# Optimization experiments

Measured on AMD Instinct MI355X. Metric: run time of the kernel, lower is better.

## Reference

```python
import jax, jax.numpy as jnp
import numpy as np

UNITS = 4096                                # number of heap nodes (power of two)
DEPTH = (UNITS - 1).bit_length() + 1        # 13 heap steps (k = 0..12)
FEATURES = [2, 64, 64, 2]
BATCH = 256


def _build_heap_maps(nodes):
    """For each heap step k, precompute for every output node j the input
    (ancestor) node index it reads from, plus a validity mask. This encodes
    exactly the torch block loop: for level l, input nodes [floor(2^(l-1)), 2^l)
    broadcast (repeat_interleave by heap_factor) into output range
    [out_node0, out_node1), with blocks where out_node1 > nodes skipped."""
    depth = (nodes - 1).bit_length() + 1
    maps = []
    for k in range(depth):
        idx = np.zeros(nodes, np.int32)
        mask = np.zeros(nodes, np.bool_)
        for l in range(depth):
            in0 = 0 if l == 0 else 2 ** (l - 1)
            if in0 == 0:  # root block (node 0)
                hf = 1 if k == 0 else 2 ** (k - 1)      # ceil(2^(k-1))
                out0 = 0 if k == 0 else 2 ** (k - 1)    # floor(2^(k-1))
                out1 = out0 + hf
            else:
                hf = 2 ** k
                out0 = in0 * hf
                out1 = (2 ** l) * hf
            if out1 <= nodes:
                js = np.arange(out0, out1)
                idx[js] = in0 + (js - out0) // hf
                mask[js] = True
        maps.append((jnp.asarray(idx), jnp.asarray(mask)))
    return maps


MAPS = _build_heap_maps(UNITS)


def heap_linear(x, W, b, minheap):
    # x: [..., nodes, in_f]; W: [K, out_f, in_f]; b: [K, out_f]; K = DEPTH - minheap
    out = jnp.zeros(x.shape[:-1] + (W.shape[1],), jnp.float32)
    for i, k in enumerate(range(minheap, DEPTH)):
        idx, mask = MAPS[k]
        # apply linear_k to every node once, then gather parent -> children
        y = jnp.einsum('...ni,oi->...no', x, W[i]) + b[i]
        out = out + jnp.where(mask[:, None], y[..., idx, :], 0.0)
    return out


def setup_inputs() -> dict:
    key = jax.random.key(0)
    ks = jax.random.split(key, 7)
    f0, f1, f2, f3 = FEATURES

    def w(k, n, o, i):
        return jax.random.normal(k, (n, o, i), jnp.float32) / np.float32(np.sqrt(i))

    return {
        "x": jax.random.normal(ks[0], (BATCH, UNITS, f0), jnp.float32),
        "W1": w(ks[1], DEPTH - 1, f1, f0),   # minheap=1 -> 12 sublayers
        "b1": jax.random.normal(ks[2], (DEPTH - 1, f1), jnp.float32) * 0.01,
        "W2": w(ks[3], DEPTH, f2, f1),       # minheap=0 -> 13 sublayers
        "b2": jax.random.normal(ks[4], (DEPTH, f2), jnp.float32) * 0.01,
        "W3": w(ks[5], DEPTH, f3, f2),
        "b3": jax.random.normal(ks[6], (DEPTH, f3), jnp.float32) * 0.01,
    }


def reference(x, W1, b1, W2, b2, W3, b3):
    h = heap_linear(x, W1, b1, minheap=1)
    h = jax.nn.relu(h)
    h = heap_linear(h, W2, b2, minheap=0)
    h = jax.nn.relu(h)
    logits = heap_linear(h, W3, b3, minheap=0)
    return logits
```

## Files before the change

kernel.cpp:

```cpp
#include <hip/hip_runtime.h>

#define UNITS 4096
#define DEPTH 13
#define BATCH 256

typedef __attribute__((ext_vector_type(8))) short s16x8;
typedef __attribute__((ext_vector_type(4))) float f32x4;
typedef __attribute__((ext_vector_type(4))) int   i32x4;

__device__ __forceinline__ unsigned short f2bf(float f){
  unsigned u = __builtin_bit_cast(unsigned, f);
  u += 0x7FFFu + ((u >> 16) & 1u);
  return (unsigned short)(u >> 16);
}
__device__ __forceinline__ int levelof(int j){ return j ? (32 - __clz(j)) : 0; }

struct FragA { s16x8 v[2]; };
struct FragB { s16x8 v[2][4]; };

__device__ __forceinline__ void load_afrag(FragA& f, const unsigned short* __restrict__ Hq,
                                           int rowbase, int l15, int kg){
  #pragma unroll
  for (int kk = 0; kk < 2; ++kk)
    f.v[kk] = *(const s16x8*)(Hq + ((size_t)((kk*4 + kg)*256 + rowbase + l15))*8);
}
__device__ __forceinline__ void load_bfrag(FragB& f, const unsigned short* __restrict__ Wf,
                                           int lane){
  #pragma unroll
  for (int kk = 0; kk < 2; ++kk)
    #pragma unroll
    for (int n = 0; n < 4; ++n)
      f.v[kk][n] = *(const s16x8*)(Wf + ((size_t)((kk*4 + n)*64 + lane))*8);
}
__device__ __forceinline__ void mstep(f32x4 acc[4], const FragA& A, const FragB& B){
  #pragma unroll
  for (int kk = 0; kk < 2; ++kk)
    #pragma unroll
    for (int n = 0; n < 4; ++n)
      acc[n] = __builtin_amdgcn_mfma_f32_16x16x32_bf16(A.v[kk], B.v[kk][n], acc[n], 0, 0, 0);
}
__device__ __forceinline__ void negA(FragA& A){
  const i32x4 sgn = {(int)0x80008000, (int)0x80008000, (int)0x80008000, (int)0x80008000};
  #pragma unroll
  for (int kk = 0; kk < 2; ++kk){
    i32x4 t = __builtin_bit_cast(i32x4, A.v[kk]);
    t ^= sgn;
    A.v[kk] = __builtin_bit_cast(s16x8, t);
  }
}

__device__ __forceinline__ float rowsum16(float s){
  int v, u;
  v = __builtin_bit_cast(int, s);
  u = __builtin_amdgcn_update_dpp(v, v, 0xB1, 0xF, 0xF, false);
  s += __builtin_bit_cast(float, u);
  v = __builtin_bit_cast(int, s);
  u = __builtin_amdgcn_update_dpp(v, v, 0x4E, 0xF, 0xF, false);
  s += __builtin_bit_cast(float, u);
  v = __builtin_bit_cast(int, s);
  u = __builtin_amdgcn_update_dpp(v, v, 0x141, 0xF, 0xF, false);
  s += __builtin_bit_cast(float, u);
  v = __builtin_bit_cast(int, s);
  u = __builtin_amdgcn_update_dpp(v, v, 0x140, 0xF, 0xF, false);
  s += __builtin_bit_cast(float, u);
  return s;
}

__device__ __forceinline__ void epilogue(const f32x4 acc[4], int p, int lp,
    const float cbv[4], const float* w3s,
    float* __restrict__ y3, int rowbase, int l15, int kg){
  int tmax = 11 - lp;
  for (int tt = 0; tt <= tmax; ++tt){
    float w30[4], w31[4];
    #pragma unroll
    for (int n = 0; n < 4; ++n){
      w30[n] = w3s[(tt*2 + 0)*64 + n*16 + l15];
      w31[n] = w3s[(tt*2 + 1)*64 + n*16 + l15];
    }
    int off = 4096 - (4096 >> tt);
    #pragma unroll
    for (int reg = 0; reg < 4; ++reg){
      float s0 = 0.f, s1 = 0.f;
      #pragma unroll
      for (int n = 0; n < 4; ++n){
        float hv = fmaxf(acc[n][reg] + cbv[n], 0.f);
        s0 = fmaf(w30[n], hv, s0);
        s1 = fmaf(w31[n], hv, s1);
      }
      s0 = rowsum16(s0);
      s1 = rowsum16(s1);
      if (l15 == 0){
        int b = rowbase + kg*4 + reg;
        float2 v; v.x = s0; v.y = s1;
        *(float2*)(y3 + ((size_t)(off + p)*256 + b)*2) = v;
      }
    }
  }
}

__global__ __launch_bounds__(256) void k_prep(const float* __restrict__ W2,
    const float* __restrict__ W1, const float* __restrict__ W3,
    const float* __restrict__ b1, const float* __restrict__ b2, const float* __restrict__ b3,
    unsigned short* __restrict__ W2f, unsigned short* __restrict__ W1f,
    float* __restrict__ cb1, float* __restrict__ cb2, float* __restrict__ cb3,
    float* __restrict__ w3h20){
  int blk = blockIdx.x, t = threadIdx.x;
  if (blk < 26){
    int u = blk*256 + t;
    int lane = u & 63, c = (u >> 6) & 7, k = u >> 9;
    int n = c & 3, kk = c >> 2, l15 = lane & 15, kg = lane >> 4;
    s16x8 rr;
    #pragma unroll
    for (int e = 0; e < 8; ++e)
      rr[e] = (short)f2bf(W2[((size_t)(k*64 + n*16 + l15))*64 + kk*32 + kg*8 + e]);
    *(s16x8*)(W2f + (size_t)u*8) = rr;
  } else if (blk == 26){
    int n = t >> 6, lane = t & 63, l15 = lane & 15, kg = lane >> 4;
    int f = n*16 + l15;
    s16x8 r = {0,0,0,0,0,0,0,0};
    #pragma unroll
    for (int j = 0; j < 4; ++j){
      int m = kg*4 + j;
      if (m < DEPTH-1){
        r[2*j]   = (short)f2bf(W1[(m*64 + f)*2]);
        r[2*j+1] = (short)f2bf(W1[(m*64 + f)*2 + 1]);
      }
    }
    *(s16x8*)(W1f + (size_t)t*8) = r;
  } else {
    if (t < 64){
      float r = 0.f;
      cb1[t] = 0.f;
      for (int m = 1; m < DEPTH; ++m){ r += b1[(m-1)*64 + t]; cb1[m*64 + t] = r; }
      float r2 = 0.f;
      for (int m = 0; m < DEPTH; ++m){ r2 += b2[m*64 + t]; cb2[m*64 + t] = r2; }
    } else if (t < 66){
      int o = t - 64;
      float r = 0.f;
      for (int m = 0; m < DEPTH; ++m){ r += b3[m*2 + o]; cb3[m*2 + o] = r; }
    } else if (t >= 128 && t < 128 + DEPTH*2){
      int q = t - 128, tt = q >> 1, o = q & 1;
      float s = 0.f;
      for (int f = 0; f < 64; ++f)
        s = fmaf(W3[(tt*2 + o)*64 + f], fmaxf(b2[f], 0.f), s);
      w3h20[tt*2 + o] = s;
    }
  }
}

__global__ __launch_bounds__(256) void k_xpose(const float* __restrict__ x,
                                               float* __restrict__ xT){
  __shared__ float2 tile[64][65];
  int jb = (blockIdx.x & 63) * 64;
  int bb = (blockIdx.x >> 6) * 64;
  int t = threadIdx.x;
  #pragma unroll
  for (int i = 0; i < 16; ++i){
    int idx = i*256 + t;
    int jj = idx & 63, b = idx >> 6;
    tile[jj][b] = *(const float2*)(x + (((size_t)(bb + b))*UNITS + jb + jj)*2);
  }
  __syncthreads();
  #pragma unroll
  for (int i = 0; i < 16; ++i){
    int idx = i*256 + t;
    int b = idx & 63, jj = idx >> 6;
    *(float2*)(xT + (((size_t)(jb + jj))*BATCH + bb + b)*2) = tile[jj][b];
  }
}

__global__ __launch_bounds__(256) void k_GH(const float* __restrict__ xT,
    const unsigned short* __restrict__ W1f, const float* __restrict__ cb1,
    unsigned short* __restrict__ H){
  __shared__ unsigned short tile[BATCH*64];
  int p = blockIdx.x;
  int lvl = levelof(p);
  int t = threadIdx.x, wid = t >> 6, lane = t & 63, l15 = lane & 15, kg = lane >> 4;

  s16x8 af[4];
  #pragma unroll
  for (int m = 0; m < 4; ++m){
    int b = wid*64 + m*16 + l15;
    s16x8 r = {0,0,0,0,0,0,0,0};
    #pragma unroll
    for (int j = 0; j < 4; ++j){
      int mm = kg*4 + j;
      if (mm <= lvl){
        float2 xv = *(const float2*)(xT + ((size_t)(p >> mm)*BATCH + b)*2);
        r[2*j]   = (short)f2bf(xv.x);
        r[2*j+1] = (short)f2bf(xv.y);
      }
    }
    af[m] = r;
  }
  f32x4 acc[4][4];
  #pragma unroll
  for (int m = 0; m < 4; ++m)
    #pragma unroll
    for (int n = 0; n < 4; ++n) acc[m][n] = (f32x4){0.f,0.f,0.f,0.f};
  #pragma unroll
  for (int n = 0; n < 4; ++n){
    s16x8 bf = *(const s16x8*)(W1f + ((size_t)n*64 + lane)*8);
    #pragma unroll
    for (int m = 0; m < 4; ++m)
      acc[m][n] = __builtin_amdgcn_mfma_f32_16x16x32_bf16(af[m], bf, acc[m][n], 0, 0, 0);
  }
  int lvl1 = lvl + 1;
  float cbv[4];
  #pragma unroll
  for (int n = 0; n < 4; ++n) cbv[n] = cb1[lvl1*64 + n*16 + l15];
  #pragma unroll
  for (int m = 0; m < 4; ++m)
    #pragma unroll
    for (int n = 0; n < 4; ++n)
      #pragma unroll
      for (int i = 0; i < 4; ++i){
        int row = wid*64 + m*16 + kg*4 + i;
        int col = n*16 + l15;
        float v = fmaxf(acc[m][n][i] + cbv[n], 0.f);
        *(unsigned short*)((char*)tile + ((row*128 + col*2) ^ ((row & 7) << 4))) = f2bf(v);
      }
  __syncthreads();
  #pragma unroll
  for (int i = 0; i < 8; ++i){
    s16x8 v = *(const s16x8*)((const char*)tile + ((t*128 + i*16) ^ ((t & 7) << 4)));
    *(s16x8*)(H + (size_t)p*16384 + ((size_t)i*256 + t)*8) = v;
  }
}

#define CHB(slot, kk) if ((kk) <= L) load_bfrag(b##slot, W2f + (size_t)(kk)*4096, lane);
#define CHA(slot, ss) if ((ss)+2 <= L) load_afrag(a##slot, H + ((size_t)(q >> (ss)))*16384, rowbase, l15, kg);
#define CHM(as, bs, ss) if ((ss)+2 <= L) mstep(acc, a##as, b##bs);

__global__ __launch_bounds__(256, 3) void k_F9(const unsigned short* __restrict__ H,
    const unsigned short* __restrict__ W2f, const float* __restrict__ cb2,
    const float* __restrict__ W3, float* __restrict__ y3){
  __shared__ float w3s[26*64];
  int bid = blockIdx.x;
  int slice = bid >> 9;
  int r   = bid & 511;
  int q   = 511 - ((r & 7)*64 + (r >> 3));
  int t = threadIdx.x, wid = t >> 6, lane = t & 63, l15 = lane & 15, kg = lane >> 4;
  int rowbase = slice*64 + wid*16;

  #pragma unroll
  for (int i = 0; i < 2; ++i){
    int idx = i*256 + t;
    if (idx < 416) ((float4*)w3s)[idx] = ((const float4*)W3)[idx];
  }
  __syncthreads();

  f32x4 acc[4];
  #pragma unroll
  for (int n = 0; n < 4; ++n) acc[n] = (f32x4){0.f, 0.f, 0.f, 0.f};

  if (q == 0){
    FragA A; FragB B;
    for (int p = 0; p < 4; ++p){
      int lp = levelof(p);
      float cbv[4];
      #pragma unroll
      for (int n = 0; n < 4; ++n) cbv[n] = cb2[(lp+1)*64 + n*16 + l15];
      #pragma unroll
      for (int n = 0; n < 4; ++n) acc[n] = (f32x4){0.f, 0.f, 0.f, 0.f};
      for (int k = 0; k <= lp; ++k){
        load_bfrag(B, W2f + (size_t)k*4096, lane);
        load_afrag(A, H + (size_t)(p >> k)*16384, rowbase, l15, kg);
        mstep(acc, A, B);
      }
      epilogue(acc, p, lp, cbv, w3s, y3, rowbase, l15, kg);
    }
    return;
  }

  const int L = levelof(q) + 2;
  float cbv[4];
  #pragma unroll
  for (int n = 0; n < 4; ++n) cbv[n] = cb2[(L+1)*64 + n*16 + l15];

  FragA a0, a1, a2; FragB b0, b1;

  CHB(0,2) CHB(1,3)
  CHA(0,0) CHA(1,1) CHA(2,2)
  CHM(0,0,0) CHB(0,4)  CHA(0,3)
  CHM(1,1,1) CHB(1,5)  CHA(1,4)
  CHM(2,0,2) CHB(0,6)  CHA(2,5)
  CHM(0,1,3) CHB(1,7)  CHA(0,6)
  CHM(1,0,4) CHB(0,8)  CHA(1,7)
  CHM(2,1,5) CHB(1,9)  CHA(2,8)
  CHM(0,0,6) CHB(0,10) CHA(0,9)
  CHM(1,1,7) CHB(1,11)
  load_afrag(a1, H + (size_t)(2*q)*16384, rowbase, l15, kg);
  CHM(2,0,8)
  load_bfrag(b0, W2f + 4096, lane);
  load_afrag(a2, H + (size_t)(4*q)*16384, rowbase, l15, kg);
  CHM(0,1,9)
  load_bfrag(b1, W2f, lane);
  load_afrag(a0, H + (size_t)(4*q + 1)*16384, rowbase, l15, kg);

  mstep(acc, a1, b0);
  mstep(acc, a2, b1);
  epilogue(acc, 4*q, L, cbv, w3s, y3, rowbase, l15, kg);
  negA(a2); mstep(acc, a2, b1);
  load_afrag(a2, H + (size_t)(2*q + 1)*16384, rowbase, l15, kg);
  mstep(acc, a0, b1);
  epilogue(acc, 4*q + 1, L, cbv, w3s, y3, rowbase, l15, kg);
  negA(a0); mstep(acc, a0, b1);
  load_afrag(a0, H + (size_t)(4*q + 2)*16384, rowbase, l15, kg);
  negA(a1); mstep(acc, a1, b0);
  load_afrag(a1, H + (size_t)(4*q + 3)*16384, rowbase, l15, kg);
  mstep(acc, a2, b0);
  mstep(acc, a0, b1);
  epilogue(acc, 4*q + 2, L, cbv, w3s, y3, rowbase, l15, kg);
  negA(a0); mstep(acc, a0, b1);
  mstep(acc, a1, b1);
  epilogue(acc, 4*q + 3, L, cbv, w3s, y3, rowbase, l15, kg);
}

__global__ __launch_bounds__(256) void k_scatter(const float* __restrict__ y3,
    const float* __restrict__ cb3, const float* __restrict__ w3h20,
    float* __restrict__ out){
  int i = blockIdx.x;
  int b = threadIdx.x;
  float4 o[4];
  #pragma unroll
  for (int c = 0; c < 4; ++c){
    int p = i*4 + c;
    int lp = levelof(p);
    float s0 = cb3[(lp+1)*2]     + w3h20[(lp+1)*2];
    float s1 = cb3[(lp+1)*2 + 1] + w3h20[(lp+1)*2 + 1];
    for (int k = 0; k <= lp; ++k){
      int pi = (4096 - (4096 >> k)) + (p >> k);
      float2 v = *(const float2*)(y3 + ((size_t)pi*256 + b)*2);
      s0 += v.x; s1 += v.y;
    }
    if (p == 0){
      o[c].x = cb3[0] + w3h20[0];
      o[c].y = cb3[1] + w3h20[1];
      o[c].z = s0; o[c].w = s1;
    } else {
      o[c].x = s0; o[c].y = s1; o[c].z = s0; o[c].w = s1;
    }
  }
  float4* dst = (float4*)(out + (size_t)b*8192 + (size_t)i*16);
  #pragma unroll
  for (int c = 0; c < 4; ++c) dst[c] = o[c];
}

extern "C" void kernel_launch(void* const* d_in, const int* in_sizes, int n_in,
                              void* d_out, int out_size, void* d_ws, size_t ws_size,
                              hipStream_t stream){
  const float* x  = (const float*)d_in[0];
  const float* W1 = (const float*)d_in[1];
  const float* b1 = (const float*)d_in[2];
  const float* W2 = (const float*)d_in[3];
  const float* b2 = (const float*)d_in[4];
  const float* W3 = (const float*)d_in[5];
  const float* b3 = (const float*)d_in[6];
  float* out = (float*)d_out;
  char* ws = (char*)d_ws;

  unsigned short* W2f   = (unsigned short*)(ws + 0);
  unsigned short* W1f   = (unsigned short*)(ws + 106496);
  float* cb1   = (float*)(ws + 110592);
  float* cb2   = (float*)(ws + 113920);
  float* cb3   = (float*)(ws + 117248);
  float* w3h20 = (float*)(ws + 117376);
  float* xT    = (float*)(ws + 117504);
  unsigned short* H = (unsigned short*)(ws + 8506112);
  float* y3    = (float*)(ws + 75614976);

  hipLaunchKernelGGL(k_prep,    dim3(28),   dim3(256), 0, stream, W2, W1, W3, b1, b2, b3, W2f, W1f, cb1, cb2, cb3, w3h20);
  hipLaunchKernelGGL(k_xpose,   dim3(256),  dim3(256), 0, stream, x, xT);
  hipLaunchKernelGGL(k_GH,      dim3(2048), dim3(256), 0, stream, xT, W1f, cb1, H);
  hipLaunchKernelGGL(k_F9,      dim3(2048), dim3(256), 0, stream, H, W2f, cb2, W3, y3);
  hipLaunchKernelGGL(k_scatter, dim3(512),  dim3(256), 0, stream, y3, cb3, w3h20, out);
}
```

Baseline: 121.1 us.

## Stage F9 operands through double-buffered LDS via async global-to-LDS loads

```diff
diff --git a/kernel.cpp b/kernel.cpp
--- a/kernel.cpp
+++ b/kernel.cpp
@@ -18,19 +18,37 @@
 struct FragA { s16x8 v[2]; };
 struct FragB { s16x8 v[2][4]; };
 
-__device__ __forceinline__ void load_afrag(FragA& f, const unsigned short* __restrict__ Hq,
-                                           int rowbase, int l15, int kg){
+__device__ __forceinline__ void gll16(const void* g, void* l){
+  __builtin_amdgcn_global_load_lds(
+      (const __attribute__((address_space(1))) unsigned int*)g,
+      (__attribute__((address_space(3))) unsigned int*)l, 16, 0, 0);
+}
+
+__device__ __forceinline__ void load_afragG(FragA& f, const unsigned short* __restrict__ Hq,
+                                            int rowbase, int l15, int kg){
   #pragma unroll
   for (int kk = 0; kk < 2; ++kk)
     f.v[kk] = *(const s16x8*)(Hq + ((size_t)((kk*4 + kg)*256 + rowbase + l15))*8);
 }
-__device__ __forceinline__ void load_bfrag(FragB& f, const unsigned short* __restrict__ Wf,
-                                           int lane){
+__device__ __forceinline__ void load_bfragG(FragB& f, const unsigned short* __restrict__ Wf,
+                                            int lane){
   #pragma unroll
   for (int kk = 0; kk < 2; ++kk)
     #pragma unroll
     for (int n = 0; n < 4; ++n)
       f.v[kk][n] = *(const s16x8*)(Wf + ((size_t)((kk*4 + n)*64 + lane))*8);
+}
+__device__ __forceinline__ void ld_afragL(FragA& f, const char* Ab, int wid, int l15, int kg){
+  #pragma unroll
+  for (int kk = 0; kk < 2; ++kk)
+    f.v[kk] = *(const s16x8*)(Ab + (kk*4 + kg)*1024 + (wid*16 + l15)*16);
+}
+__device__ __forceinline__ void ld_bfragL(FragB& f, const char* Bb, int lane){
+  #pragma unroll
+  for (int kk = 0; kk < 2; ++kk)
+    #pragma unroll
+    for (int n = 0; n < 4; ++n)
+      f.v[kk][n] = *(const s16x8*)(Bb + ((kk*4 + n)*64 + lane)*16);
 }
 __device__ __forceinline__ void mstep(f32x4 acc[4], const FragA& A, const FragB& B){
   #pragma unroll
@@ -228,33 +246,35 @@
   }
 }
 
-#define CHB(slot, kk) if ((kk) <= L) load_bfrag(b##slot, W2f + (size_t)(kk)*4096, lane);
-#define CHA(slot, ss) if ((ss)+2 <= L) load_afrag(a##slot, H + ((size_t)(q >> (ss)))*16384, rowbase, l15, kg);
-#define CHM(as, bs, ss) if ((ss)+2 <= L) mstep(acc, a##as, b##bs);
-
-__global__ __launch_bounds__(256, 3) void k_F9(const unsigned short* __restrict__ H,
+__global__ __launch_bounds__(256, 4) void k_F10(const unsigned short* __restrict__ H,
     const unsigned short* __restrict__ W2f, const float* __restrict__ cb2,
     const float* __restrict__ W3, float* __restrict__ y3){
+  __shared__ char As[2*8192];
+  __shared__ char Bs[2*8192];
   __shared__ float w3s[26*64];
+
   int bid = blockIdx.x;
   int slice = bid >> 9;
-  int r   = bid & 511;
-  int q   = 511 - ((r & 7)*64 + (r >> 3));
+  int r = bid & 511;
+  int q = 511 - ((r & 7)*64 + (r >> 3));
   int t = threadIdx.x, wid = t >> 6, lane = t & 63, l15 = lane & 15, kg = lane >> 4;
   int rowbase = slice*64 + wid*16;
+
+  const char* Hb   = (const char*)H;
+  const char* W2fb = (const char*)W2f;
 
   #pragma unroll
   for (int i = 0; i < 2; ++i){
     int idx = i*256 + t;
     if (idx < 416) ((float4*)w3s)[idx] = ((const float4*)W3)[idx];
   }
-  __syncthreads();
 
   f32x4 acc[4];
   #pragma unroll
   for (int n = 0; n < 4; ++n) acc[n] = (f32x4){0.f, 0.f, 0.f, 0.f};
 
   if (q == 0){
+    __syncthreads();
     FragA A; FragB B;
     for (int p = 0; p < 4; ++p){
       int lp = levelof(p);
@@ -264,8 +284,8 @@
       #pragma unroll
       for (int n = 0; n < 4; ++n) acc[n] = (f32x4){0.f, 0.f, 0.f, 0.f};
       for (int k = 0; k <= lp; ++k){
-        load_bfrag(B, W2f + (size_t)k*4096, lane);
-        load_afrag(A, H + (size_t)(p >> k)*16384, rowbase, l15, kg);
+        load_bfragG(B, W2f + (size_t)k*4096, lane);
+        load_afragG(A, H + (size_t)(p >> k)*16384, rowbase, l15, kg);
         mstep(acc, A, B);
       }
       epilogue(acc, p, lp, cbv, w3s, y3, rowbase, l15, kg);
@@ -274,47 +294,82 @@
   }
 
   const int L = levelof(q) + 2;
+  const int S = L + 5;
   float cbv[4];
   #pragma unroll
   for (int n = 0; n < 4; ++n) cbv[n] = cb2[(L+1)*64 + n*16 + l15];
 
-  FragA a0, a1, a2; FragB b0, b1;
-
-  CHB(0,2) CHB(1,3)
-  CHA(0,0) CHA(1,1) CHA(2,2)
-  CHM(0,0,0) CHB(0,4)  CHA(0,3)
-  CHM(1,1,1) CHB(1,5)  CHA(1,4)
-  CHM(2,0,2) CHB(0,6)  CHA(2,5)
-  CHM(0,1,3) CHB(1,7)  CHA(0,6)
-  CHM(1,0,4) CHB(0,8)  CHA(1,7)
-  CHM(2,1,5) CHB(1,9)  CHA(2,8)
-  CHM(0,0,6) CHB(0,10) CHA(0,9)
-  CHM(1,1,7) CHB(1,11)
-  load_afrag(a1, H + (size_t)(2*q)*16384, rowbase, l15, kg);
-  CHM(2,0,8)
-  load_bfrag(b0, W2f + 4096, lane);
-  load_afrag(a2, H + (size_t)(4*q)*16384, rowbase, l15, kg);
-  CHM(0,1,9)
-  load_bfrag(b1, W2f, lane);
-  load_afrag(a0, H + (size_t)(4*q + 1)*16384, rowbase, l15, kg);
-
-  mstep(acc, a1, b0);
-  mstep(acc, a2, b1);
-  epilogue(acc, 4*q, L, cbv, w3s, y3, rowbase, l15, kg);
-  negA(a2); mstep(acc, a2, b1);
-  load_afrag(a2, H + (size_t)(2*q + 1)*16384, rowbase, l15, kg);
-  mstep(acc, a0, b1);
-  epilogue(acc, 4*q + 1, L, cbv, w3s, y3, rowbase, l15, kg);
-  negA(a0); mstep(acc, a0, b1);
-  load_afrag(a0, H + (size_t)(4*q + 2)*16384, rowbase, l15, kg);
-  negA(a1); mstep(acc, a1, b0);
-  load_afrag(a1, H + (size_t)(4*q + 3)*16384, rowbase, l15, kg);
-  mstep(acc, a2, b0);
-  mstep(acc, a0, b1);
-  epilogue(acc, 4*q + 2, L, cbv, w3s, y3, rowbase, l15, kg);
-  negA(a0); mstep(acc, a0, b1);
-  mstep(acc, a1, b1);
-  epilogue(acc, 4*q + 3, L, cbv, w3s, y3, rowbase, l15, kg);
+  auto stage = [&](int u){
+    int tileA; const char* Wk;
+    if (u <= L-2){
+      tileA = q >> u;
+      Wk = W2fb + (size_t)(u+2)*8192;
+    } else {
+      int d = u - (L-1);
+      tileA = (d==0) ? 2*q : (d==1) ? 4*q : (d==2) ? 4*q+1
+            : (d==3) ? 2*q+1 : (d==4) ? 4*q+2 : 4*q+3;
+      Wk = (d==0 || d==3) ? (W2fb + 8192) : W2fb;
+    }
+    const char* Ht = Hb + (size_t)tileA*32768;
+    char* Ab = As + (u & 1)*8192;
+    char* Bb = Bs + (u & 1)*8192;
+    #pragma unroll
+    for (int j = 0; j < 2; ++j){
+      int piece = wid*2 + j;
+      gll16(Ht + piece*4096 + (slice*64 + lane)*16, Ab + piece*1024);
+    }
+    #pragma unroll
+    for (int j = 0; j < 2; ++j){
+      int c = wid*2 + j;
+      gll16(Wk + c*1024 + lane*16, Bb + c*1024);
+    }
+  };
+
+  stage(0);
+  __syncthreads();
+
+  FragA held0, held1;
+
+  for (int s = 0; s < S; ++s){
+    if (s + 1 < S) stage(s + 1);
+    const char* Ab = As + (s & 1)*8192;
+    const char* Bb = Bs + (s & 1)*8192;
+    FragB bF; ld_bfragL(bF, Bb, lane);
+    if (s <= L-2){
+      FragA aF; ld_afragL(aF, Ab, wid, l15, kg);
+      mstep(acc, aF, bF);
+    } else {
+      int d = s - (L-1);
+      if (d == 0){
+        ld_afragL(held0, Ab, wid, l15, kg);
+        mstep(acc, held0, bF);
+      } else if (d == 1){
+        ld_afragL(held1, Ab, wid, l15, kg);
+        mstep(acc, held1, bF);
+        epilogue(acc, 4*q, L, cbv, w3s, y3, rowbase, l15, kg);
+      } else if (d == 2){
+        negA(held1); mstep(acc, held1, bF);
+        ld_afragL(held1, Ab, wid, l15, kg);
+        mstep(acc, held1, bF);
+        epilogue(acc, 4*q + 1, L, cbv, w3s, y3, rowbase, l15, kg);
+      } else if (d == 3){
+        negA(held0); mstep(acc, held0, bF);
+        FragA aF; ld_afragL(aF, Ab, wid, l15, kg);
+        mstep(acc, aF, bF);
+      } else if (d == 4){
+        negA(held1); mstep(acc, held1, bF);
+        ld_afragL(held1, Ab, wid, l15, kg);
+        mstep(acc, held1, bF);
+        epilogue(acc, 4*q + 2, L, cbv, w3s, y3, rowbase, l15, kg);
+      } else {
+        negA(held1); mstep(acc, held1, bF);
+        FragA aF; ld_afragL(aF, Ab, wid, l15, kg);
+        mstep(acc, aF, bF);
+        epilogue(acc, 4*q + 3, L, cbv, w3s, y3, rowbase, l15, kg);
+      }
+    }
+    __syncthreads();
+  }
 }
 
 __global__ __launch_bounds__(256) void k_scatter(const float* __restrict__ y3,
@@ -373,6 +428,6 @@
   hipLaunchKernelGGL(k_prep,    dim3(28),   dim3(256), 0, stream, W2, W1, W3, b1, b2, b3, W2f, W1f, cb1, cb2, cb3, w3h20);
   hipLaunchKernelGGL(k_xpose,   dim3(256),  dim3(256), 0, stream, x, xT);
   hipLaunchKernelGGL(k_GH,      dim3(2048), dim3(256), 0, stream, xT, W1f, cb1, H);
-  hipLaunchKernelGGL(k_F9,      dim3(2048), dim3(256), 0, stream, H, W2f, cb2, W3, y3);
+  hipLaunchKernelGGL(k_F10,     dim3(2048), dim3(256), 0, stream, H, W2f, cb2, W3, y3);
   hipLaunchKernelGGL(k_scatter, dim3(512),  dim3(256), 0, stream, y3, cb3, w3h20, out);
 }
```

New measurement: 176.0 us. 45.3% more time.
